# Optimization experiments

Measured on AMD Instinct MI355X. Metric: run time of the kernel, lower is better.

The kernel has to match this reference:

```python
import jax, jax.numpy as jnp
import numpy as np

H = 64          # HIDDEN_DIM
V = 64          # VOCAB_SIZE
THR = 0.4       # ENERGY_THRESHOLD
LN_EPS = 1e-5
NORM_EPS = 1e-12


def _layer_norm(x, g, b):
    mu = jnp.mean(x, axis=-1, keepdims=True)
    var = jnp.var(x, axis=-1, keepdims=True)
    return (x - mu) * jax.lax.rsqrt(var + LN_EPS) * g + b


def setup_inputs() -> dict:
    key = jax.random.key(0)
    ks = jax.random.split(key, 12)
    B, L = 256, 2048
    s = 0.05
    return {
        "x": jax.random.randint(ks[0], (B, L), 0, V),
        "embed": jax.random.normal(ks[1], (V, H), jnp.float32) * s,
        "w1": jax.random.normal(ks[2], (H, 2 * H), jnp.float32) * s,
        "b1": jnp.zeros((2 * H,), jnp.float32),
        "w2": jax.random.normal(ks[3], (2 * H, H), jnp.float32) * s,
        "b2": jnp.zeros((H,), jnp.float32),
        "ln_g": jnp.ones((H,), jnp.float32),
        "ln_b": jnp.zeros((H,), jnp.float32),
        "wk": jax.random.normal(ks[4], (H, H), jnp.float32) * s,
        "wv": jax.random.normal(ks[5], (H, H), jnp.float32) * s,
        "wq": jax.random.normal(ks[6], (H, H), jnp.float32) * s,
        "wo": jax.random.normal(ks[7], (H, V), jnp.float32) * s,
        "bo": jnp.zeros((V,), jnp.float32),
    }


def reference(x, embed, w1, b1, w2, b2, ln_g, ln_b, wk, wv, wq, wo, bo):
    # Encoder: embed -> FFN -> residual -> LayerNorm
    h = embed[x]                                        # [B, L, H]
    ff = jax.nn.relu(h @ w1 + b1) @ w2 + b2
    h = _layer_norm(h + ff, ln_g, ln_b)                 # [B, L, H]

    B = h.shape[0]
    # Precompute all k (L2-normalized) and v projections, then scan over time.
    k = h @ wk                                          # [B, L, H]
    k = k / jnp.maximum(jnp.linalg.norm(k, axis=-1, keepdims=True), NORM_EPS)
    v = h @ wv                                          # [B, L, H]

    def step(M, kv):
        k_t, v_t = kv                                   # each [B, H]
        pred = jnp.einsum('bij,bj->bi', M, k_t)         # [B, H]
        delta = v_t - pred
        gate = (jnp.linalg.norm(delta, axis=-1, keepdims=True)
                > THR * jnp.linalg.norm(v_t, axis=-1, keepdims=True)).astype(M.dtype)
        M = M + gate[:, :, None] * jnp.einsum('bi,bj->bij', delta, k_t)
        return M, None

    M0 = jnp.zeros((B, H, H), h.dtype)
    M, _ = jax.lax.scan(step, M0,
                        (jnp.swapaxes(k, 0, 1), jnp.swapaxes(v, 0, 1)))

    q = h[:, -1, :] @ wq                                # [B, H]
    read = jax.nn.relu(jnp.einsum('bij,bj->bi', M, q))  # [B, H]
    return read @ wo + bo                               # [B, V]
```

## Files before the change

kernel.cpp:

```cpp
#include <hip/hip_runtime.h>
#include <hip/hip_bf16.h>

#define HD   64
#define SEQ  2048
#define NB   256
#define TWOH 128
#define NCH  32

typedef float v4f __attribute__((ext_vector_type(4)));


#define WS_V    4096
#define WS_Q    8192
#define WS_THR  12288
#define WS_FLAG 12352

template <int CTRL>
__device__ __forceinline__ float dpp_add(float x) {
    int y = __builtin_amdgcn_update_dpp(0, __builtin_bit_cast(int, x),
                                        CTRL, 0xF, 0xF, true);
    return x + __builtin_bit_cast(float, y);
}

__device__ __forceinline__ float wave_total(float x) {
    x = dpp_add<0x111>(x);
    x = dpp_add<0x112>(x);
    x = dpp_add<0x114>(x);
    x = dpp_add<0x118>(x);
    x = dpp_add<0x142>(x);
    x = dpp_add<0x143>(x);
    return __builtin_bit_cast(float,
        __builtin_amdgcn_readlane(__builtin_bit_cast(int, x), 63));
}

__device__ __forceinline__ float bcastf(float v, int l) {
    return __builtin_bit_cast(float,
        __builtin_amdgcn_readlane(__builtin_bit_cast(int, v), l));
}

__device__ __forceinline__ float hsum4(v4f a) {
    return (a.x + a.y) + (a.z + a.w);
}

__device__ __forceinline__ bool detect_bf16(const void* embed) {
    const unsigned short* u = (const unsigned short*)embed;
    int bad = 0;
    for (int i = 2 * threadIdx.x; i < 4096; i += 128) {
        float v = __uint_as_float(((unsigned int)u[i]) << 16);
        if (!(fabsf(v) < 1e4f)) bad = 1;
    }
    return !__any(bad);
}

template <bool BF>
__device__ __forceinline__ float ldf(const void* p, int i) {
    if (BF) return __bfloat162float(((const __hip_bfloat16*)p)[i]);
    return ((const float*)p)[i];
}

template <bool BF>
__device__ void precompute_body(const void* embed, const void* w1, const void* b1,
                                const void* w2, const void* b2, const void* ln_g,
                                const void* ln_b, const void* wk, const void* wv,
                                const void* wq, float* __restrict__ ws) {
    const int t = blockIdx.x, d = threadIdx.x;
    __shared__ float sh_h[HD];
    __shared__ float sh_u[TWOH];

    float h = ldf<BF>(embed, t * HD + d);
    sh_h[d] = h;
    __syncthreads();

    float a0 = 0.f, a1 = 0.f, a2 = 0.f, a3 = 0.f;
    #pragma unroll 16
    for (int j = 0; j < HD; j += 2) {
        float h0 = sh_h[j], h1 = sh_h[j + 1];
        a0 = fmaf(h0, ldf<BF>(w1, j * TWOH + d), a0);
        a1 = fmaf(h0, ldf<BF>(w1, j * TWOH + d + HD), a1);
        a2 = fmaf(h1, ldf<BF>(w1, (j + 1) * TWOH + d), a2);
        a3 = fmaf(h1, ldf<BF>(w1, (j + 1) * TWOH + d + HD), a3);
    }
    float u0 = fmaxf(a0 + a2 + ldf<BF>(b1, d), 0.f);
    float u1 = fmaxf(a1 + a3 + ldf<BF>(b1, d + HD), 0.f);
    sh_u[d] = u0;
    sh_u[d + HD] = u1;
    __syncthreads();

    float f0 = 0.f, f1 = 0.f, f2 = 0.f, f3 = 0.f;
    #pragma unroll 16
    for (int e = 0; e < TWOH; e += 4) {
        f0 = fmaf(sh_u[e + 0], ldf<BF>(w2, (e + 0) * HD + d), f0);
        f1 = fmaf(sh_u[e + 1], ldf<BF>(w2, (e + 1) * HD + d), f1);
        f2 = fmaf(sh_u[e + 2], ldf<BF>(w2, (e + 2) * HD + d), f2);
        f3 = fmaf(sh_u[e + 3], ldf<BF>(w2, (e + 3) * HD + d), f3);
    }
    float y = h + (f0 + f1) + (f2 + f3) + ldf<BF>(b2, d);

    float mu  = wave_total(y) * 0.015625f;
    float dvv = y - mu;
    float var = wave_total(dvv * dvv) * 0.015625f;
    float hn  = fmaf(dvv * (1.f / sqrtf(var + 1e-5f)), ldf<BF>(ln_g, d),
                     ldf<BF>(ln_b, d));

    __syncthreads();
    sh_h[d] = hn;
    __syncthreads();

    float k0 = 0.f, k1 = 0.f, v0 = 0.f, v1 = 0.f, q0 = 0.f, q1 = 0.f;
    #pragma unroll 16
    for (int j = 0; j < HD; j += 2) {
        float h0 = sh_h[j], h1 = sh_h[j + 1];
        k0 = fmaf(h0, ldf<BF>(wk, j * HD + d), k0);
        v0 = fmaf(h0, ldf<BF>(wv, j * HD + d), v0);
        q0 = fmaf(h0, ldf<BF>(wq, j * HD + d), q0);
        k1 = fmaf(h1, ldf<BF>(wk, (j + 1) * HD + d), k1);
        v1 = fmaf(h1, ldf<BF>(wv, (j + 1) * HD + d), v1);
        q1 = fmaf(h1, ldf<BF>(wq, (j + 1) * HD + d), q1);
    }
    float k = k0 + k1, v = v0 + v1, q = q0 + q1;
    float nk = sqrtf(wave_total(k * k));
    k /= fmaxf(nk, 1e-12f);
    float nv2 = wave_total(v * v);

    ws[t * HD + d]        = k;
    ws[WS_V + t * HD + d] = v;
    ws[WS_Q + t * HD + d] = q;
    if (d == 0) ws[WS_THR + t] = 0.16f * nv2;
    if (t == 0 && d == 0) ws[WS_FLAG] = BF ? 1.f : 0.f;
}

__global__ __launch_bounds__(64) void precompute_kernel(
    const void* embed, const void* w1, const void* b1, const void* w2,
    const void* b2, const void* ln_g, const void* ln_b, const void* wk,
    const void* wv, const void* wq, float* __restrict__ ws) {
    if (detect_bf16(embed))
        precompute_body<true>(embed, w1, b1, w2, b2, ln_g, ln_b, wk, wv, wq, ws);
    else
        precompute_body<false>(embed, w1, b1, w2, b2, ln_g, ln_b, wk, wv, wq, ws);
}

__global__ __launch_bounds__(256, 1) void scan_kernel(
    const int* __restrict__ x, const float* __restrict__ ws,
    const void* __restrict__ wo, const void* __restrict__ bo,
    void* __restrict__ out) {
    const int b = blockIdx.x, tid = threadIdx.x;
    const int wv = tid >> 6, lane = tid & 63;
    __shared__ __align__(16) float k_lds[4096];
    __shared__ __align__(16) float g_lds[4096];
    __shared__ int   tok_lds[SEQ];
    __shared__ float pbuf[2][4][64];
    __shared__ __align__(16) float rd_lds[64];

    #pragma unroll
    for (int i = 0; i < 4; ++i) {
        int o = i * 1024 + tid * 4;
        *(float4*)&k_lds[o] = *(const float4*)&ws[o];
    }
    const int* xr = x + b * SEQ;
    #pragma unroll
    for (int c = 0; c < 8; ++c) tok_lds[c * 256 + tid] = xr[c * 256 + tid];

    const float thr2 = ws[WS_THR + lane];
    const bool  bf   = ws[WS_FLAG] != 0.f;

    v4f kreg[16];
    const float* krow = ws + lane * HD;
    #pragma unroll
    for (int i = 0; i < 16; ++i) {
        float4 kv = *(const float4*)&krow[i * 4];
        kreg[i] = (v4f){kv.x, kv.y, kv.z, kv.w};
    }
    const int tl = xr[SEQ - 1];
    const float* qrow = ws + WS_Q + tl * HD;
    v4f cacc = {0.f, 0.f, 0.f, 0.f};
    #pragma unroll
    for (int i = 0; i < 16; ++i) {
        const float* qp = &qrow[i * 4];
        v4f qv = {qp[0], qp[1], qp[2], qp[3]};
        cacc = __builtin_elementwise_fma(qv, kreg[i], cacc);
    }
    const float cq = hsum4(cacc);
    __syncthreads();

    #pragma unroll 1
    for (int t0 = 0; t0 < 16; ++t0) {
        const int t = wv * 16 + t0;
        const float* kt = &k_lds[t * HD];
        v4f a = {0.f, 0.f, 0.f, 0.f};
        #pragma unroll
        for (int i = 0; i < 16; ++i) {
            const v4f kv = *(const v4f*)&kt[i * 4];
            a = __builtin_elementwise_fma(kv, kreg[i], a);
        }
        g_lds[t * HD + lane] = hsum4(a);
    }

    v4f dv[4], R[4];
    const float* vr = ws + WS_V + lane * HD + wv * 16;
    v4f acc = {0.f, 0.f, 0.f, 0.f};
    #pragma unroll
    for (int i = 0; i < 4; ++i) {
        float4 vvv = *(const float4*)&vr[i * 4];
        dv[i] = (v4f){vvv.x, vvv.y, vvv.z, vvv.w};
        R[i]  = (v4f){0.f, 0.f, 0.f, 0.f};
        acc   = __builtin_elementwise_fma(dv[i], dv[i], acc);
    }
    pbuf[0][wv][lane] = hsum4(acc);
    int pp = 1;
    __syncthreads();
    float nd2 = ((pbuf[0][0][lane] + pbuf[0][1][lane]) +
                 (pbuf[0][2][lane] + pbuf[0][3][lane]));
    unsigned long long fireset = __ballot(nd2 > thr2);

    int chunk = tok_lds[lane];
    #pragma unroll 1
    for (int c = 0; c < NCH; ++c) {
        int nxt = 0;
        if (c + 1 < NCH) nxt = tok_lds[(c + 1) * 64 + lane];
        unsigned long long pend = __ballot((int)((fireset >> chunk) & 1ull));
        while (pend) {
            const int s = __builtin_ctzll(pend);
            const int t = __builtin_amdgcn_readlane(chunk, s);
            const float g   = g_lds[t * HD + lane];
            const float cqt = bcastf(cq, t);
            const v4f gs  = {-g, -g, -g, -g};
            const v4f cqs = {cqt, cqt, cqt, cqt};
            v4f q4 = {0.f, 0.f, 0.f, 0.f};
            #pragma unroll
            for (int i = 0; i < 4; ++i) {
                v4f sve;
                sve.x = bcastf(dv[i].x, t);
                sve.y = bcastf(dv[i].y, t);
                sve.z = bcastf(dv[i].z, t);
                sve.w = bcastf(dv[i].w, t);
                dv[i] = __builtin_elementwise_fma(gs, sve, dv[i]);
                R[i]  = __builtin_elementwise_fma(cqs, sve, R[i]);
                q4    = __builtin_elementwise_fma(dv[i], dv[i], q4);
            }
            pbuf[pp][wv][lane] = hsum4(q4);
            __syncthreads();
            nd2 = ((pbuf[pp][0][lane] + pbuf[pp][1][lane]) +
                   (pbuf[pp][2][lane] + pbuf[pp][3][lane]));
            pp ^= 1;
            fireset = __ballot(nd2 > thr2);
            const unsigned long long above =
                (s >= 63) ? 0ull : (~0ull << (s + 1));
            pend = __ballot((int)((fireset >> chunk) & 1ull)) & above;
        }
        chunk = nxt;
    }

    if (lane == 0) {
        #pragma unroll
        for (int i = 0; i < 4; ++i) {
            v4f r = R[i];
            r.x = fmaxf(r.x, 0.f); r.y = fmaxf(r.y, 0.f);
            r.z = fmaxf(r.z, 0.f); r.w = fmaxf(r.w, 0.f);
            *(v4f*)&rd_lds[wv * 16 + i * 4] = r;
        }
    }
    __syncthreads();

    if (wv == 0) {
        if (bf) {
            float acc2 = __bfloat162float(((const __hip_bfloat16*)bo)[lane]);
            #pragma unroll 8
            for (int j = 0; j < HD; ++j)
                acc2 = fmaf(rd_lds[j],
                    __bfloat162float(((const __hip_bfloat16*)wo)[j * HD + lane]),
                    acc2);
            ((__hip_bfloat16*)out)[b * HD + lane] = __float2bfloat16(acc2);
        } else {
            float acc2 = ((const float*)bo)[lane];
            #pragma unroll 8
            for (int j = 0; j < HD; ++j)
                acc2 = fmaf(rd_lds[j], ((const float*)wo)[j * HD + lane], acc2);
            ((float*)out)[b * HD + lane] = acc2;
        }
    }
}

extern "C" void kernel_launch(void* const* d_in, const int* in_sizes, int n_in,
                              void* d_out, int out_size, void* d_ws, size_t ws_size,
                              hipStream_t stream) {
    const int* x      = (const int*)d_in[0];
    const void* embed = d_in[1];
    const void* w1    = d_in[2];
    const void* b1    = d_in[3];
    const void* w2    = d_in[4];
    const void* b2    = d_in[5];
    const void* ln_g  = d_in[6];
    const void* ln_b  = d_in[7];
    const void* wk    = d_in[8];
    const void* wv    = d_in[9];
    const void* wq    = d_in[10];
    const void* wo    = d_in[11];
    const void* bo    = d_in[12];
    float* ws = (float*)d_ws;

    precompute_kernel<<<64, 64, 0, stream>>>(embed, w1, b1, w2, b2, ln_g, ln_b,
                                             wk, wv, wq, ws);
    scan_kernel<<<NB, 256, 0, stream>>>(x, ws, wo, bo, d_out);
}
```

Baseline: 284.2 us.

## Fuse vocab precompute into scan kernel, recomputing per block in LDS

Removes the separate 64-block precompute kernel and its global workspace round-trip. Each of the 256 scan blocks now redundantly encodes all 64 vocabulary tokens (FFN, LayerNorm, k/v/q projections), one wave per 16 tokens, writing results straight into LDS. This saves a kernel launch and the dependency between kernels, but multiplies the encoder work by the number of blocks and raises LDS use by about 32 KB per block.

```diff
diff --git a/kernel.cpp b/kernel.cpp
--- a/kernel.cpp
+++ b/kernel.cpp
@@ -8,12 +8,6 @@
 #define NCH  32
 
 typedef float v4f __attribute__((ext_vector_type(4)));
-
-
-#define WS_V    4096
-#define WS_Q    8192
-#define WS_THR  12288
-#define WS_FLAG 12352
 
 template <int CTRL>
 __device__ __forceinline__ float dpp_add(float x) {
@@ -42,10 +36,10 @@
     return (a.x + a.y) + (a.z + a.w);
 }
 
-__device__ __forceinline__ bool detect_bf16(const void* embed) {
+__device__ __forceinline__ bool detect_bf16(const void* embed, int lane) {
     const unsigned short* u = (const unsigned short*)embed;
     int bad = 0;
-    for (int i = 2 * threadIdx.x; i < 4096; i += 128) {
+    for (int i = 2 * lane; i < 4096; i += 128) {
         float v = __uint_as_float(((unsigned int)u[i]) << 16);
         if (!(fabsf(v) < 1e4f)) bad = 1;
     }
@@ -59,132 +53,126 @@
 }
 
 template <bool BF>
-__device__ void precompute_body(const void* embed, const void* w1, const void* b1,
-                                const void* w2, const void* b2, const void* ln_g,
-                                const void* ln_b, const void* wk, const void* wv,
-                                const void* wq, float* __restrict__ ws) {
-    const int t = blockIdx.x, d = threadIdx.x;
-    __shared__ float sh_h[HD];
-    __shared__ float sh_u[TWOH];
-
-    float h = ldf<BF>(embed, t * HD + d);
-    sh_h[d] = h;
-    __syncthreads();
-
-    float a0 = 0.f, a1 = 0.f, a2 = 0.f, a3 = 0.f;
-    #pragma unroll 16
-    for (int j = 0; j < HD; j += 2) {
-        float h0 = sh_h[j], h1 = sh_h[j + 1];
-        a0 = fmaf(h0, ldf<BF>(w1, j * TWOH + d), a0);
-        a1 = fmaf(h0, ldf<BF>(w1, j * TWOH + d + HD), a1);
-        a2 = fmaf(h1, ldf<BF>(w1, (j + 1) * TWOH + d), a2);
-        a3 = fmaf(h1, ldf<BF>(w1, (j + 1) * TWOH + d + HD), a3);
-    }
-    float u0 = fmaxf(a0 + a2 + ldf<BF>(b1, d), 0.f);
-    float u1 = fmaxf(a1 + a3 + ldf<BF>(b1, d + HD), 0.f);
-    sh_u[d] = u0;
-    sh_u[d + HD] = u1;
-    __syncthreads();
-
-    float f0 = 0.f, f1 = 0.f, f2 = 0.f, f3 = 0.f;
-    #pragma unroll 16
-    for (int e = 0; e < TWOH; e += 4) {
-        f0 = fmaf(sh_u[e + 0], ldf<BF>(w2, (e + 0) * HD + d), f0);
-        f1 = fmaf(sh_u[e + 1], ldf<BF>(w2, (e + 1) * HD + d), f1);
-        f2 = fmaf(sh_u[e + 2], ldf<BF>(w2, (e + 2) * HD + d), f2);
-        f3 = fmaf(sh_u[e + 3], ldf<BF>(w2, (e + 3) * HD + d), f3);
-    }
-    float y = h + (f0 + f1) + (f2 + f3) + ldf<BF>(b2, d);
-
-    float mu  = wave_total(y) * 0.015625f;
-    float dvv = y - mu;
-    float var = wave_total(dvv * dvv) * 0.015625f;
-    float hn  = fmaf(dvv * (1.f / sqrtf(var + 1e-5f)), ldf<BF>(ln_g, d),
-                     ldf<BF>(ln_b, d));
-
-    __syncthreads();
-    sh_h[d] = hn;
-    __syncthreads();
-
-    float k0 = 0.f, k1 = 0.f, v0 = 0.f, v1 = 0.f, q0 = 0.f, q1 = 0.f;
-    #pragma unroll 16
-    for (int j = 0; j < HD; j += 2) {
-        float h0 = sh_h[j], h1 = sh_h[j + 1];
-        k0 = fmaf(h0, ldf<BF>(wk, j * HD + d), k0);
-        v0 = fmaf(h0, ldf<BF>(wv, j * HD + d), v0);
-        q0 = fmaf(h0, ldf<BF>(wq, j * HD + d), q0);
-        k1 = fmaf(h1, ldf<BF>(wk, (j + 1) * HD + d), k1);
-        v1 = fmaf(h1, ldf<BF>(wv, (j + 1) * HD + d), v1);
-        q1 = fmaf(h1, ldf<BF>(wq, (j + 1) * HD + d), q1);
-    }
-    float k = k0 + k1, v = v0 + v1, q = q0 + q1;
-    float nk = sqrtf(wave_total(k * k));
-    k /= fmaxf(nk, 1e-12f);
-    float nv2 = wave_total(v * v);
-
-    ws[t * HD + d]        = k;
-    ws[WS_V + t * HD + d] = v;
-    ws[WS_Q + t * HD + d] = q;
-    if (d == 0) ws[WS_THR + t] = 0.16f * nv2;
-    if (t == 0 && d == 0) ws[WS_FLAG] = BF ? 1.f : 0.f;
-}
-
-__global__ __launch_bounds__(64) void precompute_kernel(
-    const void* embed, const void* w1, const void* b1, const void* w2,
-    const void* b2, const void* ln_g, const void* ln_b, const void* wk,
-    const void* wv, const void* wq, float* __restrict__ ws) {
-    if (detect_bf16(embed))
-        precompute_body<true>(embed, w1, b1, w2, b2, ln_g, ln_b, wk, wv, wq, ws);
-    else
-        precompute_body<false>(embed, w1, b1, w2, b2, ln_g, ln_b, wk, wv, wq, ws);
-}
-
-__global__ __launch_bounds__(256, 1) void scan_kernel(
-    const int* __restrict__ x, const float* __restrict__ ws,
-    const void* __restrict__ wo, const void* __restrict__ bo,
-    void* __restrict__ out) {
+__device__ void encode16(int wid, int lane, const void* embed, const void* w1,
+                         const void* b1, const void* w2, const void* b2,
+                         const void* ln_g, const void* ln_b, const void* wk,
+                         const void* wvp, const void* wq,
+                         float* __restrict__ k_lds, float* __restrict__ v_lds,
+                         float* __restrict__ q_lds, float* __restrict__ thr2_lds,
+                         float* __restrict__ shh, float* __restrict__ shu) {
+    #pragma unroll 1
+    for (int it = 0; it < 16; ++it) {
+        const int t = wid * 16 + it;
+        float h = ldf<BF>(embed, t * HD + lane);
+        shh[lane] = h;
+        asm volatile("s_waitcnt lgkmcnt(0)" ::: "memory");
+
+        float a0 = 0.f, a1 = 0.f, a2 = 0.f, a3 = 0.f;
+        #pragma unroll 16
+        for (int j = 0; j < HD; j += 2) {
+            float h0 = shh[j], h1 = shh[j + 1];
+            a0 = fmaf(h0, ldf<BF>(w1, j * TWOH + lane), a0);
+            a1 = fmaf(h0, ldf<BF>(w1, j * TWOH + lane + HD), a1);
+            a2 = fmaf(h1, ldf<BF>(w1, (j + 1) * TWOH + lane), a2);
+            a3 = fmaf(h1, ldf<BF>(w1, (j + 1) * TWOH + lane + HD), a3);
+        }
+        shu[lane]      = fmaxf(a0 + a2 + ldf<BF>(b1, lane), 0.f);
+        shu[lane + HD] = fmaxf(a1 + a3 + ldf<BF>(b1, lane + HD), 0.f);
+        asm volatile("s_waitcnt lgkmcnt(0)" ::: "memory");
+
+        float f0 = 0.f, f1 = 0.f, f2 = 0.f, f3 = 0.f;
+        #pragma unroll 16
+        for (int e = 0; e < TWOH; e += 4) {
+            f0 = fmaf(shu[e + 0], ldf<BF>(w2, (e + 0) * HD + lane), f0);
+            f1 = fmaf(shu[e + 1], ldf<BF>(w2, (e + 1) * HD + lane), f1);
+            f2 = fmaf(shu[e + 2], ldf<BF>(w2, (e + 2) * HD + lane), f2);
+            f3 = fmaf(shu[e + 3], ldf<BF>(w2, (e + 3) * HD + lane), f3);
+        }
+        float y = h + (f0 + f1) + (f2 + f3) + ldf<BF>(b2, lane);
+
+        float mu  = wave_total(y) * 0.015625f;
+        float dvv = y - mu;
+        float var = wave_total(dvv * dvv) * 0.015625f;
+        float hn  = fmaf(dvv * (1.f / sqrtf(var + 1e-5f)), ldf<BF>(ln_g, lane),
+                         ldf<BF>(ln_b, lane));
+
+        shh[lane] = hn;
+        asm volatile("s_waitcnt lgkmcnt(0)" ::: "memory");
+
+        float k0 = 0.f, k1 = 0.f, v0 = 0.f, v1 = 0.f, q0 = 0.f, q1 = 0.f;
+        #pragma unroll 16
+        for (int j = 0; j < HD; j += 2) {
+            float h0 = shh[j], h1 = shh[j + 1];
+            k0 = fmaf(h0, ldf<BF>(wk, j * HD + lane), k0);
+            v0 = fmaf(h0, ldf<BF>(wvp, j * HD + lane), v0);
+            q0 = fmaf(h0, ldf<BF>(wq, j * HD + lane), q0);
+            k1 = fmaf(h1, ldf<BF>(wk, (j + 1) * HD + lane), k1);
+            v1 = fmaf(h1, ldf<BF>(wvp, (j + 1) * HD + lane), v1);
+            q1 = fmaf(h1, ldf<BF>(wq, (j + 1) * HD + lane), q1);
+        }
+        float k = k0 + k1, v = v0 + v1, q = q0 + q1;
+        float nk = sqrtf(wave_total(k * k));
+        k /= fmaxf(nk, 1e-12f);
+        float nv2 = wave_total(v * v);
+
+        k_lds[t * HD + lane] = k;
+        v_lds[t * HD + lane] = v;
+        q_lds[t * HD + lane] = q;
+        if (lane == 0) thr2_lds[t] = 0.16f * nv2;
+    }
+}
+
+__global__ __launch_bounds__(256, 1) void fused_kernel(
+    const int* __restrict__ x, const void* embed, const void* w1,
+    const void* b1, const void* w2, const void* b2, const void* ln_g,
+    const void* ln_b, const void* wk, const void* wvp, const void* wq,
+    const void* wo, const void* bo, void* __restrict__ out) {
     const int b = blockIdx.x, tid = threadIdx.x;
-    const int wv = tid >> 6, lane = tid & 63;
+    const int wid = tid >> 6, lane = tid & 63;
     __shared__ __align__(16) float k_lds[4096];
     __shared__ __align__(16) float g_lds[4096];
+    __shared__ __align__(16) float v_lds[4096];
+    __shared__ __align__(16) float q_lds[4096];
     __shared__ int   tok_lds[SEQ];
+    __shared__ float thr2_lds[64];
     __shared__ float pbuf[2][4][64];
     __shared__ __align__(16) float rd_lds[64];
-
-    #pragma unroll
-    for (int i = 0; i < 4; ++i) {
-        int o = i * 1024 + tid * 4;
-        *(float4*)&k_lds[o] = *(const float4*)&ws[o];
-    }
+    __shared__ float sh_h[4][HD];
+    __shared__ float sh_u[4][TWOH];
+
     const int* xr = x + b * SEQ;
     #pragma unroll
     for (int c = 0; c < 8; ++c) tok_lds[c * 256 + tid] = xr[c * 256 + tid];
 
-    const float thr2 = ws[WS_THR + lane];
-    const bool  bf   = ws[WS_FLAG] != 0.f;
+    const bool bf = detect_bf16(embed, lane);
+    if (bf)
+        encode16<true>(wid, lane, embed, w1, b1, w2, b2, ln_g, ln_b, wk, wvp,
+                       wq, k_lds, v_lds, q_lds, thr2_lds, sh_h[wid], sh_u[wid]);
+    else
+        encode16<false>(wid, lane, embed, w1, b1, w2, b2, ln_g, ln_b, wk, wvp,
+                        wq, k_lds, v_lds, q_lds, thr2_lds, sh_h[wid], sh_u[wid]);
+    __syncthreads();
+
+    const float thr2 = thr2_lds[lane];
 
     v4f kreg[16];
-    const float* krow = ws + lane * HD;
+    #pragma unroll
+    for (int i = 0; i < 16; ++i)
+        kreg[i] = *(const v4f*)&k_lds[lane * HD + i * 4];
+
+    const int tl = tok_lds[SEQ - 1];
+    v4f cacc = {0.f, 0.f, 0.f, 0.f};
     #pragma unroll
     for (int i = 0; i < 16; ++i) {
-        float4 kv = *(const float4*)&krow[i * 4];
-        kreg[i] = (v4f){kv.x, kv.y, kv.z, kv.w};
-    }
-    const int tl = xr[SEQ - 1];
-    const float* qrow = ws + WS_Q + tl * HD;
-    v4f cacc = {0.f, 0.f, 0.f, 0.f};
-    #pragma unroll
-    for (int i = 0; i < 16; ++i) {
-        const float* qp = &qrow[i * 4];
+        const float* qp = &q_lds[tl * HD + i * 4];
         v4f qv = {qp[0], qp[1], qp[2], qp[3]};
         cacc = __builtin_elementwise_fma(qv, kreg[i], cacc);
     }
     const float cq = hsum4(cacc);
-    __syncthreads();
 
     #pragma unroll 1
     for (int t0 = 0; t0 < 16; ++t0) {
-        const int t = wv * 16 + t0;
+        const int t = wid * 16 + t0;
         const float* kt = &k_lds[t * HD];
         v4f a = {0.f, 0.f, 0.f, 0.f};
         #pragma unroll
@@ -196,16 +184,14 @@
     }
 
     v4f dv[4], R[4];
-    const float* vr = ws + WS_V + lane * HD + wv * 16;
     v4f acc = {0.f, 0.f, 0.f, 0.f};
     #pragma unroll
     for (int i = 0; i < 4; ++i) {
-        float4 vvv = *(const float4*)&vr[i * 4];
-        dv[i] = (v4f){vvv.x, vvv.y, vvv.z, vvv.w};
+        dv[i] = *(const v4f*)&v_lds[lane * HD + wid * 16 + i * 4];
         R[i]  = (v4f){0.f, 0.f, 0.f, 0.f};
         acc   = __builtin_elementwise_fma(dv[i], dv[i], acc);
     }
-    pbuf[0][wv][lane] = hsum4(acc);
+    pbuf[0][wid][lane] = hsum4(acc);
     int pp = 1;
     __syncthreads();
     float nd2 = ((pbuf[0][0][lane] + pbuf[0][1][lane]) +
@@ -237,7 +223,7 @@
                 R[i]  = __builtin_elementwise_fma(cqs, sve, R[i]);
                 q4    = __builtin_elementwise_fma(dv[i], dv[i], q4);
             }
-            pbuf[pp][wv][lane] = hsum4(q4);
+            pbuf[pp][wid][lane] = hsum4(q4);
             __syncthreads();
             nd2 = ((pbuf[pp][0][lane] + pbuf[pp][1][lane]) +
                    (pbuf[pp][2][lane] + pbuf[pp][3][lane]));
@@ -256,12 +242,12 @@
             v4f r = R[i];
             r.x = fmaxf(r.x, 0.f); r.y = fmaxf(r.y, 0.f);
             r.z = fmaxf(r.z, 0.f); r.w = fmaxf(r.w, 0.f);
-            *(v4f*)&rd_lds[wv * 16 + i * 4] = r;
+            *(v4f*)&rd_lds[wid * 16 + i * 4] = r;
         }
     }
     __syncthreads();
 
-    if (wv == 0) {
+    if (wid == 0) {
         if (bf) {
             float acc2 = __bfloat162float(((const __hip_bfloat16*)bo)[lane]);
             #pragma unroll 8
@@ -292,13 +278,11 @@
     const void* ln_g  = d_in[6];
     const void* ln_b  = d_in[7];
     const void* wk    = d_in[8];
-    const void* wv    = d_in[9];
+    const void* wvp   = d_in[9];
     const void* wq    = d_in[10];
     const void* wo    = d_in[11];
     const void* bo    = d_in[12];
-    float* ws = (float*)d_ws;
-
-    precompute_kernel<<<64, 64, 0, stream>>>(embed, w1, b1, w2, b2, ln_g, ln_b,
-                                             wk, wv, wq, ws);
-    scan_kernel<<<NB, 256, 0, stream>>>(x, ws, wo, bo, d_out);
-}
+
+    fused_kernel<<<NB, 256, 0, stream>>>(x, embed, w1, b1, w2, b2, ln_g, ln_b,
+                                         wk, wvp, wq, wo, bo, d_out);
+}
```

New measurement: 319.1 us. +12.3%, slower.
